# Performance work log

Measured on AMD Instinct MI355X. Metric: run time of the kernel, lower is better.

Reference implementation:

```python
import jax, jax.numpy as jnp
import numpy as np

D = 1024

def setup_inputs() -> dict:
    key = jax.random.key(0)
    ks = jax.random.split(key, 12)
    B, N, d = 4, 4096, D
    init_std = 0.02 / np.sqrt(d)  # matches _init_weights for value_proj / o_proj
    inp = {
        "h": jax.random.normal(ks[0], (B, N, d), dtype=jnp.float32),
        # relation_encoder: Linear(d, d//2) -> GELU -> Linear(d//2, 1)  (weights stored [in, out])
        "W_re1": jax.random.normal(ks[1], (d, d // 2), dtype=jnp.float32) * 0.02,
        "b_re1": jnp.zeros((d // 2,), dtype=jnp.float32),
        "W_re2": jax.random.normal(ks[2], (d // 2, 1), dtype=jnp.float32) * 0.02,
        "b_re2": jnp.zeros((1,), dtype=jnp.float32),
        # value_proj: Linear(d, d, bias=False), init std = 0.02/sqrt(d)
        "W_v": jax.random.normal(ks[3], (d, d), dtype=jnp.float32) * init_std,
        # relation_transform: Linear(2d, d) -> GELU -> Linear(d, d)
        "W_rt1": jax.random.normal(ks[4], (2 * d, d), dtype=jnp.float32) * 0.02,
        "b_rt1": jnp.zeros((d,), dtype=jnp.float32),
        "W_rt2": jax.random.normal(ks[5], (d, d), dtype=jnp.float32) * 0.02,
        "b_rt2": jnp.zeros((d,), dtype=jnp.float32),
        # o_proj: Linear(d, d, bias=False), init std = 0.02/sqrt(d)
        "W_o": jax.random.normal(ks[6], (d, d), dtype=jnp.float32) * init_std,
    }
    return inp


def reference(h, W_re1, b_re1, W_re2, b_re2, W_v, W_rt1, b_rt1, W_rt2, b_rt2, W_o):
    B, N, d = h.shape
    # relation_encoder MLP -> scalar logit per token (torch GELU is exact erf form)
    hidden = jax.nn.gelu(jnp.einsum('bnd,dk->bnk', h, W_re1) + b_re1, approximate=False)
    relation_logits = (jnp.einsum('bnk,ko->bno', hidden, W_re2) + b_re2)[..., 0]  # [B, N]
    relation_strength = jax.nn.sigmoid(relation_logits)  # [B, N]
    # pointer targets: round(sigmoid * (N-1)) clamped (jnp.round == torch.round, half-to-even)
    relation_targets = jnp.clip(
        jnp.round(relation_strength * (N - 1)).astype(jnp.int32), 0, N - 1
    )  # [B, N]
    # per-token gather of target hidden state within each batch row
    target_features = jnp.take_along_axis(h, relation_targets[..., None], axis=1)  # [B, N, d]
    source_values = jnp.einsum('bnd,de->bne', h, W_v)
    target_values = jnp.einsum('bnd,de->bne', target_features, W_v)
    relation_input = jnp.concatenate([source_values, target_values], axis=-1)  # [B, N, 2d]
    relation_output = jax.nn.gelu(
        jnp.einsum('bnf,fe->bne', relation_input, W_rt1) + b_rt1, approximate=False
    )
    relation_output = jnp.einsum('bne,ef->bnf', relation_output, W_rt2) + b_rt2
    z = jnp.einsum('bnd,de->bne', relation_output, W_o)  # [B, N, d]
    return (z, relation_targets, relation_strength)
```

## Files before the change

kernel.cpp:

```cpp
#include <hip/hip_runtime.h>
#include <math.h>
#include <type_traits>

#define DMODEL 1024
#define NSEQ   4096
#define MTOT   16384

typedef unsigned short ushortT;
typedef __attribute__((ext_vector_type(8))) short short8;
typedef __attribute__((ext_vector_type(4))) float f32x4;

__device__ __forceinline__ float gelu_f(float x) {
    return 0.5f * x * (1.0f + erff(x * 0.70710678118654752440f));
}
__device__ __forceinline__ double gelu_d(double x) {
    return 0.5 * x * (1.0 + erf(x * 0.70710678118654752440));
}
__device__ __forceinline__ ushortT f2bf(float f) {
    unsigned u = __float_as_uint(f);
    u += 0x7FFFu + ((u >> 16) & 1u);
    return (ushortT)(u >> 16);
}
__device__ __forceinline__ float bf2f(ushortT b) {
    return __uint_as_float(((unsigned)b) << 16);
}
__device__ __forceinline__ void gload16(const void* g, void* l) {
    __builtin_amdgcn_global_load_lds(
        (const __attribute__((address_space(1))) unsigned*)g,
        (__attribute__((address_space(3))) unsigned*)l, 16, 0, 0);
}

enum { EPI_BIAS_F32 = 2, EPI_TRANS_BF16 = 3, EPI_PQ = 5 };

__device__ __forceinline__ int swz_off(int row, int slot) {
    return row * 64 + (((slot ^ (row & 7)) & 7) << 3);
}

template<int EPI, int NXT>
__global__ __launch_bounds__(512, 2)
void pipe_gemm(const ushortT* __restrict__ A, const ushortT* __restrict__ Bt,
               const float* __restrict__ bias, void* __restrict__ Cv,
               void* __restrict__ Cv2, int K, int lda, int ldb, int ldc, int cpx)
{
    __shared__ ushortT smem[4 * 16384];
    const int tid  = threadIdx.x;
    const int lane = tid & 63;
    const int w    = tid >> 6;
    const int wr   = w >> 2;
    const int wc   = w & 3;
    const int flat = blockIdx.x + blockIdx.y * NXT;
    const int swz  = (flat & 7) * cpx + (flat >> 3);
    const int n0   = (swz & (NXT - 1)) * 256;
    const int m0   = (swz / NXT) * 256;

    const int srow  = tid >> 3;
    const int sscol = (((tid & 7) ^ (srow & 7)) & 7) << 3;

#define STG_A(buf, q, k0) gload16(A  + (size_t)(m0 + (q)*64 + srow) * lda + (k0) + sscol, \
                                  (char*)smem + (buf)*32768 + (q)*8192 + w*1024)
#define STG_B(buf, q, k0) gload16(Bt + (size_t)(n0 + (q)*64 + srow) * ldb + (k0) + sscol, \
                                  (char*)smem + 65536 + (buf)*32768 + (q)*8192 + w*1024)
#define BAR() asm volatile("s_barrier" ::: "memory")

    f32x4 acc[8][4];
    #pragma unroll
    for (int i = 0; i < 8; i++)
        #pragma unroll
        for (int j = 0; j < 4; j++) acc[i][j] = (f32x4){0.f, 0.f, 0.f, 0.f};

    const int NT = K >> 6;

    #pragma unroll
    for (int q = 0; q < 4; q++) { STG_A(0, q, 0); STG_B(0, q, 0); }

    const int mi = lane & 15;
    const int g4 = lane >> 4;

    for (int t = 0; t < NT; ++t) {
        const int c  = t & 1;
        const int nb = c ^ 1;
        const int kn = (t + 1) << 6;
        const bool hn = (t + 1 < NT);

        if (hn) {
            STG_A(nb, 0, kn); STG_A(nb, 1, kn);
            asm volatile("s_waitcnt vmcnt(2)" ::: "memory");
        } else {
            asm volatile("s_waitcnt vmcnt(0)" ::: "memory");
        }
        BAR();

        short8 bf[4][2];
        #pragma unroll
        for (int nf = 0; nf < 4; nf++)
            #pragma unroll
            for (int ks = 0; ks < 2; ks++)
                bf[nf][ks] = *(const short8*)&smem[32768 + c * 16384 +
                                swz_off(wc * 64 + nf * 16 + mi, ks * 4 + g4)];

        #pragma unroll
        for (int p = 0; p < 4; p++) {
            if (p > 0) {
                if (hn) {
                    if (p == 1) { STG_A(nb, 2, kn); STG_A(nb, 3, kn); }
                    if (p == 2) { STG_B(nb, 0, kn); STG_B(nb, 1, kn); }
                    if (p == 3) { STG_B(nb, 2, kn); STG_B(nb, 3, kn); }
                }
                BAR();
            }
            short8 af[2][2];
            #pragma unroll
            for (int ii = 0; ii < 2; ii++)
                #pragma unroll
                for (int ks = 0; ks < 2; ks++)
                    af[ii][ks] = *(const short8*)&smem[c * 16384 +
                                    swz_off(wr * 128 + (p * 2 + ii) * 16 + mi, ks * 4 + g4)];
            __builtin_amdgcn_s_setprio(1);
            #pragma unroll
            for (int ks = 0; ks < 2; ks++)
                #pragma unroll
                for (int ii = 0; ii < 2; ii++)
                    #pragma unroll
                    for (int nf = 0; nf < 4; nf++)
                        acc[p * 2 + ii][nf] = __builtin_amdgcn_mfma_f32_16x16x32_bf16(
                            af[ii][ks], bf[nf][ks], acc[p * 2 + ii][nf], 0, 0, 0);
            __builtin_amdgcn_s_setprio(0);
        }
        BAR();
    }

    const int cr = (lane >> 4) * 4;
    #pragma unroll
    for (int i = 0; i < 8; i++) {
        #pragma unroll
        for (int j = 0; j < 4; j++) {
            const int gr = m0 + wr * 128 + i * 16 + cr;
            const int gc = n0 + wc * 64 + j * 16 + mi;
            #pragma unroll
            for (int r = 0; r < 4; r++) {
                float v = acc[i][j][r];
                if constexpr (EPI == EPI_BIAS_F32) {
                    ((float*)Cv)[(size_t)(gr + r) * ldc + gc] = v + bias[gc];
                } else {
                    if (gc < 1024)
                        ((float*)Cv)[(size_t)(gr + r) * ldc + gc] = v + bias[gc];
                    else
                        ((ushortT*)Cv2)[(size_t)(gr + r) * ldc + (gc - 1024)] = f2bf(v);
                }
            }
        }
    }
#undef STG_A
#undef STG_B
#undef BAR
}

template<int EPI, int NXT>
__global__ __launch_bounds__(256)
void mfma_gemm(const ushortT* __restrict__ A, const ushortT* __restrict__ Bt,
               const float* __restrict__ bias, void* __restrict__ Cv,
               void* __restrict__ Cv2, int K, int lda, int ldb, int ldc, int cpx)
{
    __shared__ ushortT As[128 * 32];
    __shared__ ushortT Bs[128 * 32];
    const int tid  = threadIdx.x;
    const int lane = tid & 63;
    const int w    = tid >> 6;
    const int wr   = (w >> 1) * 64;
    const int wc   = (w & 1) * 64;
    const int flat = blockIdx.x + blockIdx.y * NXT;
    const int swz  = (flat & 7) * cpx + (flat >> 3);
    const int n0   = (swz & (NXT - 1)) * 128;
    const int m0   = (swz / NXT) * 128;

    const int lrow = lane >> 2;
    const int lk   = (lane & 3) * 8;

    f32x4 acc[4][4];
    #pragma unroll
    for (int i = 0; i < 4; i++)
        #pragma unroll
        for (int j = 0; j < 4; j++) acc[i][j] = (f32x4){0.f, 0.f, 0.f, 0.f};

    for (int kk = 0; kk < K; kk += 32) {
        #pragma unroll
        for (int i = 0; i < 2; i++) {
            const ushortT* ga = A + (size_t)(m0 + w * 32 + i * 16 + lrow) * lda + kk + lk;
            gload16(ga, &As[(w * 32 + i * 16) * 32]);
            const ushortT* gb = Bt + (size_t)(n0 + w * 32 + i * 16 + lrow) * ldb + kk + lk;
            gload16(gb, &Bs[(w * 32 + i * 16) * 32]);
        }
        __syncthreads();

        const int mi = lane & 15;
        const int ko = (lane >> 4) * 8;
        short8 a[4], b[4];
        #pragma unroll
        for (int i = 0; i < 4; i++)
            a[i] = *(const short8*)&As[(wr + i * 16 + mi) * 32 + ko];
        #pragma unroll
        for (int j = 0; j < 4; j++)
            b[j] = *(const short8*)&Bs[(wc + j * 16 + mi) * 32 + ko];
        #pragma unroll
        for (int i = 0; i < 4; i++)
            #pragma unroll
            for (int j = 0; j < 4; j++)
                acc[i][j] = __builtin_amdgcn_mfma_f32_16x16x32_bf16(a[i], b[j], acc[i][j], 0, 0, 0);
        __syncthreads();
    }

    const int cr = (lane >> 4) * 4;
    const int cc = lane & 15;
    #pragma unroll
    for (int i = 0; i < 4; i++) {
        #pragma unroll
        for (int j = 0; j < 4; j++) {
            const int gr = m0 + wr + i * 16 + cr;
            const int gc = n0 + wc + j * 16 + cc;
            #pragma unroll
            for (int r = 0; r < 4; r++) {
                float v = acc[i][j][r];
                if constexpr (EPI == EPI_BIAS_F32)
                    ((float*)Cv)[(size_t)(gr + r) * ldc + gc] = v + bias[gc];
                else
                    ((ushortT*)Cv)[(size_t)gc * ldc + (gr + r)] = f2bf(v);
            }
        }
    }
}

__global__ __launch_bounds__(256)
void gelu_gather_k(const float* __restrict__ P, const ushortT* __restrict__ Q,
                   const int* __restrict__ gidx, ushortT* __restrict__ G)
{
    const int m = blockIdx.x;
    int t = gidx[m];
    t = max(0, min(t, MTOT - 1));
    const int c = threadIdx.x * 4;
    float4 p = *(const float4*)(P + (size_t)m * DMODEL + c);
    ushort4 q = *(const ushort4*)(Q + (size_t)t * DMODEL + c);
    ushortT o[4];
    o[0] = f2bf(gelu_f(p.x + bf2f(q.x)));
    o[1] = f2bf(gelu_f(p.y + bf2f(q.y)));
    o[2] = f2bf(gelu_f(p.z + bf2f(q.z)));
    o[3] = f2bf(gelu_f(p.w + bf2f(q.w)));
    *(ulong1*)(G + (size_t)m * DMODEL + c) = *(ulong1*)o;
}

__global__ __launch_bounds__(256)
void wsplit_gemm(const ushortT* __restrict__ Ah, const ushortT* __restrict__ Al,
                 const ushortT* __restrict__ Bh0, const ushortT* __restrict__ Bl0,
                 ushortT* __restrict__ Ct0, int K, int lda, int ldb, int ldc)
{
    __shared__ ushortT Ash[128 * 32], Asl[128 * 32];
    __shared__ ushortT Bsh[128 * 32], Bsl[128 * 32];
    const int tid  = threadIdx.x;
    const int lane = tid & 63;
    const int w    = tid >> 6;
    const int wr   = (w >> 1) * 64;
    const int wc   = (w & 1) * 64;
    const int sel  = blockIdx.y >> 3;
    const int m0   = (blockIdx.y & 7) * 128;
    const int n0   = blockIdx.x * 128;
    const ushortT* Bh = Bh0 + sel * 1024;
    const ushortT* Bl = Bl0 + sel * 1024;
    ushortT* Ct = Ct0 + (size_t)sel * 1024 * 1024;
    const int lrow = lane >> 2;
    const int lk   = (lane & 3) * 8;

    f32x4 acc[4][4];
    #pragma unroll
    for (int i = 0; i < 4; i++)
        #pragma unroll
        for (int j = 0; j < 4; j++) acc[i][j] = (f32x4){0.f, 0.f, 0.f, 0.f};

    for (int kk = 0; kk < K; kk += 32) {
        #pragma unroll
        for (int i = 0; i < 2; i++) {
            const size_t aoff = (size_t)(m0 + w * 32 + i * 16 + lrow) * lda + kk + lk;
            const size_t boff = (size_t)(n0 + w * 32 + i * 16 + lrow) * ldb + kk + lk;
            const int ldst = (w * 32 + i * 16) * 32;
            gload16(Ah + aoff, &Ash[ldst]);
            gload16(Al + aoff, &Asl[ldst]);
            gload16(Bh + boff, &Bsh[ldst]);
            gload16(Bl + boff, &Bsl[ldst]);
        }
        __syncthreads();

        const int mi = lane & 15;
        const int ko = (lane >> 4) * 8;
        short8 ah[4], al[4], bh[4], bl[4];
        #pragma unroll
        for (int i = 0; i < 4; i++) {
            ah[i] = *(const short8*)&Ash[(wr + i * 16 + mi) * 32 + ko];
            al[i] = *(const short8*)&Asl[(wr + i * 16 + mi) * 32 + ko];
        }
        #pragma unroll
        for (int j = 0; j < 4; j++) {
            bh[j] = *(const short8*)&Bsh[(wc + j * 16 + mi) * 32 + ko];
            bl[j] = *(const short8*)&Bsl[(wc + j * 16 + mi) * 32 + ko];
        }
        #pragma unroll
        for (int i = 0; i < 4; i++)
            #pragma unroll
            for (int j = 0; j < 4; j++) {
                acc[i][j] = __builtin_amdgcn_mfma_f32_16x16x32_bf16(ah[i], bh[j], acc[i][j], 0, 0, 0);
                acc[i][j] = __builtin_amdgcn_mfma_f32_16x16x32_bf16(ah[i], bl[j], acc[i][j], 0, 0, 0);
                acc[i][j] = __builtin_amdgcn_mfma_f32_16x16x32_bf16(al[i], bh[j], acc[i][j], 0, 0, 0);
            }
        __syncthreads();
    }

    const int cr = (lane >> 4) * 4;
    const int cc = lane & 15;
    #pragma unroll
    for (int i = 0; i < 4; i++)
        #pragma unroll
        for (int j = 0; j < 4; j++) {
            const int gr = m0 + wr + i * 16 + cr;
            const int gc = n0 + wc + j * 16 + cc;
            #pragma unroll
            for (int r = 0; r < 4; r++)
                Ct[(size_t)gc * ldc + (gr + r)] = f2bf(acc[i][j][r]);
        }
}

__global__ __launch_bounds__(256)
void enc_gemm(const ushortT* __restrict__ Ah, const ushortT* __restrict__ Al,
              const ushortT* __restrict__ Bh, const ushortT* __restrict__ Bl,
              const float* __restrict__ bias, float* __restrict__ C)
{
    __shared__ ushortT Ash[128 * 32], Asl[128 * 32];
    __shared__ ushortT Bsh[128 * 32], Bsl[128 * 32];
    const int tid  = threadIdx.x;
    const int lane = tid & 63;
    const int w    = tid >> 6;
    const int wr   = (w >> 1) * 64;
    const int wc   = (w & 1) * 64;
    const int flat = blockIdx.x + (blockIdx.y << 2);
    const int swz  = (flat & 7) * 64 + (flat >> 3);
    const int n0   = (swz & 3) * 128;
    const int m0   = (swz >> 2) * 128;
    const int lrow = lane >> 2;
    const int lk   = (lane & 3) * 8;

    f32x4 acc[4][4];
    #pragma unroll
    for (int i = 0; i < 4; i++)
        #pragma unroll
        for (int j = 0; j < 4; j++) acc[i][j] = (f32x4){0.f, 0.f, 0.f, 0.f};

    for (int kk = 0; kk < DMODEL; kk += 32) {
        #pragma unroll
        for (int i = 0; i < 2; i++) {
            const size_t aoff = (size_t)(m0 + w * 32 + i * 16 + lrow) * DMODEL + kk + lk;
            const size_t boff = (size_t)(n0 + w * 32 + i * 16 + lrow) * DMODEL + kk + lk;
            const int ldst = (w * 32 + i * 16) * 32;
            gload16(Ah + aoff, &Ash[ldst]);
            gload16(Al + aoff, &Asl[ldst]);
            gload16(Bh + boff, &Bsh[ldst]);
            gload16(Bl + boff, &Bsl[ldst]);
        }
        __syncthreads();

        const int mi = lane & 15;
        const int ko = (lane >> 4) * 8;
        short8 ah[4], al[4], bh[4], bl[4];
        #pragma unroll
        for (int i = 0; i < 4; i++) {
            ah[i] = *(const short8*)&Ash[(wr + i * 16 + mi) * 32 + ko];
            al[i] = *(const short8*)&Asl[(wr + i * 16 + mi) * 32 + ko];
        }
        #pragma unroll
        for (int j = 0; j < 4; j++) {
            bh[j] = *(const short8*)&Bsh[(wc + j * 16 + mi) * 32 + ko];
            bl[j] = *(const short8*)&Bsl[(wc + j * 16 + mi) * 32 + ko];
        }
        #pragma unroll
        for (int i = 0; i < 4; i++)
            #pragma unroll
            for (int j = 0; j < 4; j++) {
                acc[i][j] = __builtin_amdgcn_mfma_f32_16x16x32_bf16(ah[i], bh[j], acc[i][j], 0, 0, 0);
                acc[i][j] = __builtin_amdgcn_mfma_f32_16x16x32_bf16(ah[i], bl[j], acc[i][j], 0, 0, 0);
                acc[i][j] = __builtin_amdgcn_mfma_f32_16x16x32_bf16(al[i], bh[j], acc[i][j], 0, 0, 0);
            }
        __syncthreads();
    }

    const int cr = (lane >> 4) * 4;
    const int cc = lane & 15;
    #pragma unroll
    for (int i = 0; i < 4; i++)
        #pragma unroll
        for (int j = 0; j < 4; j++) {
            const int gr = m0 + wr + i * 16 + cr;
            const int gc = n0 + wc + j * 16 + cc;
            #pragma unroll
            for (int r = 0; r < 4; r++)
                C[(size_t)(gr + r) * 512 + gc] = gelu_f(acc[i][j][r] + bias[gc]);
        }
}

__global__ __launch_bounds__(256)
void target2_k(const float* __restrict__ Genc, const float* __restrict__ W2,
               const float* __restrict__ b2, float* __restrict__ outT,
               float* __restrict__ outS, int* __restrict__ gidx,
               int* __restrict__ cnt, int* __restrict__ list)
{
    const int m = blockIdx.x * 4 + (threadIdx.x >> 6);
    const int lane = threadIdx.x & 63;
    const float* gr = Genc + (size_t)m * 512;
    double s = 0.0;
    #pragma unroll 4
    for (int j = lane; j < 512; j += 64) s = fma((double)gr[j], (double)W2[j], s);
    #pragma unroll
    for (int off = 32; off; off >>= 1) s += __shfl_down(s, off);
    if (lane == 0) {
        double logit = s + (double)b2[0];
        double str = 1.0 / (1.0 + exp(-logit));
        double r = str * (double)(NSEQ - 1);
        double n = rint(r);
        double dist = fabs(r - n);
        n = fmin(fmax(n, 0.0), (double)(NSEQ - 1));
        int t = (int)n;
        outT[m] = (float)t;
        outS[m] = (float)str;
        gidx[m] = ((m >> 12) << 12) + t;
        if (dist > 0.46) {
            int ix = atomicAdd(cnt, 1) & (MTOT - 1);
            list[ix] = m;
        }
    }
}

#define FIX_T 4
__global__ __launch_bounds__(256)
void fixup_k(const float* __restrict__ h, const float* __restrict__ W1,
             const float* __restrict__ b1, const float* __restrict__ W2,
             const float* __restrict__ b2, const int* __restrict__ cnt_p,
             const int* __restrict__ list, float* __restrict__ outT,
             float* __restrict__ outS, int* __restrict__ gidx)
{
    __shared__ float hrow[FIX_T][1024];
    __shared__ double red[4][FIX_T];
    const int tid = threadIdx.x;
    const int cnt = min(*cnt_p, MTOT);
    for (int base = (int)blockIdx.x * FIX_T; base < cnt;
         base += (int)gridDim.x * FIX_T) {
        const int nt = min(FIX_T, cnt - base);
        for (int t = 0; t < nt; t++) {
            const int m = list[base + t];
            const float4* src = (const float4*)(h + (size_t)m * 1024);
            ((float4*)hrow[t])[tid] = src[tid];
        }
        __syncthreads();

        double a[FIX_T][2];
        #pragma unroll
        for (int t = 0; t < FIX_T; t++) { a[t][0] = 0.0; a[t][1] = 0.0; }

        #pragma unroll 4
        for (int k = 0; k < 1024; k++) {
            const double wa = (double)W1[(size_t)k * 512 + tid];
            const double wb = (double)W1[(size_t)k * 512 + tid + 256];
            #pragma unroll
            for (int t = 0; t < FIX_T; t++) {
                const double hv = (double)hrow[t][k];
                a[t][0] = fma(hv, wa, a[t][0]);
                a[t][1] = fma(hv, wb, a[t][1]);
            }
        }

        const double w2a = (double)W2[tid], w2b = (double)W2[tid + 256];
        const double b1a = (double)b1[tid], b1b = (double)b1[tid + 256];
        const int lane = tid & 63, w = tid >> 6;
        #pragma unroll
        for (int t = 0; t < FIX_T; t++) {
            double v = w2a * gelu_d(a[t][0] + b1a) + w2b * gelu_d(a[t][1] + b1b);
            #pragma unroll
            for (int off = 32; off; off >>= 1) v += __shfl_down(v, off);
            if (lane == 0) red[w][t] = v;
        }
        __syncthreads();
        if (tid < nt) {
            const int t = tid;
            double logit = red[0][t] + red[1][t] + red[2][t] + red[3][t] + (double)b2[0];
            double str = 1.0 / (1.0 + exp(-logit));
            double r = str * (double)(NSEQ - 1);
            double n = rint(r);
            n = fmin(fmax(n, 0.0), (double)(NSEQ - 1));
            const int m = list[base + t];
            const int ti = (int)n;
            outT[m] = (float)ti;
            outS[m] = (float)str;
            gidx[m] = ((m >> 12) << 12) + ti;
        }
        __syncthreads();
    }
}

__global__ __launch_bounds__(256)
void biascomb_k(const float* __restrict__ brt2, const float* __restrict__ Wo,
                float* __restrict__ bc)
{
    int j = blockIdx.x * 256 + threadIdx.x;
    float s = 0.f;
    for (int e = 0; e < DMODEL; e++) s = fmaf(brt2[e], Wo[e * DMODEL + j], s);
    bc[j] = s;
}

__global__ __launch_bounds__(256)
void cast_k(const float* __restrict__ x, ushortT* __restrict__ y, int n)
{
    int i = (blockIdx.x * 256 + threadIdx.x) * 4;
    if (i < n) {
        float4 v = *(const float4*)(x + i);
        ushortT o[4] = { f2bf(v.x), f2bf(v.y), f2bf(v.z), f2bf(v.w) };
        *(ulong1*)&y[i] = *(ulong1*)o;
    }
}

__global__ __launch_bounds__(256)
void split_cast_k(const float* __restrict__ x, ushortT* __restrict__ yh,
                  ushortT* __restrict__ yl, int n)
{
    int i = (blockIdx.x * 256 + threadIdx.x) * 4;
    if (i < n) {
        float4 v = *(const float4*)(x + i);
        float vv[4] = { v.x, v.y, v.z, v.w };
        ushortT oh[4], ol[4];
        #pragma unroll
        for (int q = 0; q < 4; q++) {
            oh[q] = f2bf(vv[q]);
            ol[q] = f2bf(vv[q] - bf2f(oh[q]));
        }
        *(ulong1*)&yh[i] = *(ulong1*)oh;
        *(ulong1*)&yl[i] = *(ulong1*)ol;
    }
}

__global__ __launch_bounds__(256)
void transcast_k(const float* __restrict__ W, ushortT* __restrict__ Wt, int K, int N)
{
    __shared__ float t[32][33];
    const int tx = threadIdx.x & 31, ty = threadIdx.x >> 5;
    const int n0 = blockIdx.x * 32, k0 = blockIdx.y * 32;
    #pragma unroll
    for (int r = 0; r < 32; r += 8)
        t[ty + r][tx] = W[(size_t)(k0 + ty + r) * N + n0 + tx];
    __syncthreads();
    #pragma unroll
    for (int r = 0; r < 32; r += 8)
        Wt[(size_t)(n0 + ty + r) * K + k0 + tx] = f2bf(t[tx][ty + r]);
}

__global__ __launch_bounds__(256)
void split_transcast_k(const float* __restrict__ W, ushortT* __restrict__ Wth,
                       ushortT* __restrict__ Wtl, int K, int N)
{
    __shared__ float t[32][33];
    const int tx = threadIdx.x & 31, ty = threadIdx.x >> 5;
    const int n0 = blockIdx.x * 32, k0 = blockIdx.y * 32;
    #pragma unroll
    for (int r = 0; r < 32; r += 8)
        t[ty + r][tx] = W[(size_t)(k0 + ty + r) * N + n0 + tx];
    __syncthreads();
    #pragma unroll
    for (int r = 0; r < 32; r += 8) {
        float x = t[tx][ty + r];
        ushortT hi = f2bf(x);
        Wth[(size_t)(n0 + ty + r) * K + k0 + tx] = hi;
        Wtl[(size_t)(n0 + ty + r) * K + k0 + tx] = f2bf(x - bf2f(hi));
    }
}

extern "C" void kernel_launch(void* const* d_in, const int* in_sizes, int n_in,
                              void* d_out, int out_size, void* d_ws, size_t ws_size,
                              hipStream_t stream)
{
    const float* h     = (const float*)d_in[0];
    const float* W_re1 = (const float*)d_in[1];
    const float* b_re1 = (const float*)d_in[2];
    const float* W_re2 = (const float*)d_in[3];
    const float* b_re2 = (const float*)d_in[4];
    const float* W_v   = (const float*)d_in[5];
    const float* W_rt1 = (const float*)d_in[6];
    const float* b_rt1 = (const float*)d_in[7];
    const float* W_rt2 = (const float*)d_in[8];
    const float* b_rt2 = (const float*)d_in[9];
    const float* W_o   = (const float*)d_in[10];

    float* z    = (float*)d_out;
    float* outT = z + (size_t)MTOT * DMODEL;
    float* outS = outT + MTOT;
    ushortT* Q    = (ushortT*)z;
    ushortT* h_hi = (ushortT*)z + (size_t)MTOT * DMODEL;

    char* ws = (char*)d_ws;
    ushortT* G       = (ushortT*)ws;
    float*   Genc    = (float*)(ws + (32ull  << 20));
    ushortT* h_lo    = (ushortT*)(ws + (64ull  << 20));
    float*   P       = (float*)(ws + (32ull  << 20));
    ushortT* Wrt1t_h = (ushortT*)(ws + (96ull  << 20));
    ushortT* Wrt1t_l = (ushortT*)(ws + (100ull << 20));
    ushortT* Wv_h    = (ushortT*)(ws + (104ull << 20));
    ushortT* Wv_l    = (ushortT*)(ws + (106ull << 20));
    ushortT* Wa_t    = (ushortT*)(ws + (108ull << 20));
    ushortT* Wo_t    = (ushortT*)(ws + (112ull << 20));
    ushortT* Wrt2_b  = (ushortT*)(ws + (114ull << 20));
    ushortT* Wc_t    = (ushortT*)(ws + (116ull << 20));
    ushortT* Wre1t_h = (ushortT*)(ws + (118ull << 20));
    ushortT* Wre1t_l = (ushortT*)(ws + (119ull << 20));
    float*   b_c     = (float*)(ws + (120ull << 20));
    int*     cnt     = (int*)  (ws + (120ull << 20) + 4096);
    int*     gidx    = (int*)  (ws + (120ull << 20) + 8192);
    int*     list    = (int*)  (ws + (120ull << 20) + 8192 + 65536);

    split_cast_k<<<dim3(MTOT * DMODEL / 1024), 256, 0, stream>>>(h, h_hi, h_lo, MTOT * DMODEL);
    split_cast_k<<<dim3(DMODEL * DMODEL / 1024), 256, 0, stream>>>(W_v, Wv_h, Wv_l, DMODEL * DMODEL);
    split_transcast_k<<<dim3(16, 32), 256, 0, stream>>>(W_re1, Wre1t_h, Wre1t_l, DMODEL, 512);
    split_transcast_k<<<dim3(32, 64), 256, 0, stream>>>(W_rt1, Wrt1t_h, Wrt1t_l, 2 * DMODEL, DMODEL);
    cast_k<<<dim3(DMODEL * DMODEL / 1024), 256, 0, stream>>>(W_rt2, Wrt2_b, DMODEL * DMODEL);
    transcast_k<<<dim3(32, 32), 256, 0, stream>>>(W_o, Wo_t, DMODEL, DMODEL);
    biascomb_k<<<dim3(4), 256, 0, stream>>>(b_rt2, W_o, b_c);

    wsplit_gemm<<<dim3(8, 16), 256, 0, stream>>>(Wv_h, Wv_l, Wrt1t_h, Wrt1t_l,
                                                 Wa_t, DMODEL, DMODEL, 2 * DMODEL, DMODEL);

    enc_gemm<<<dim3(4, 128), 256, 0, stream>>>(h_hi, h_lo, Wre1t_h, Wre1t_l, b_re1, Genc);

    hipMemsetAsync(cnt, 0, 4, stream);
    target2_k<<<dim3(MTOT / 4), 256, 0, stream>>>(Genc, W_re2, b_re2, outT, outS, gidx, cnt, list);
    fixup_k<<<dim3(4096), 256, 0, stream>>>(h, W_re1, b_re1, W_re2, b_re2, cnt, list,
                                            outT, outS, gidx);

    mfma_gemm<EPI_TRANS_BF16, 8><<<dim3(8, 8), 256, 0, stream>>>(
        Wrt2_b, Wo_t, nullptr, (void*)Wc_t, nullptr, DMODEL, DMODEL, DMODEL, DMODEL, 8);

    pipe_gemm<EPI_PQ, 8><<<dim3(8, 64), 512, 0, stream>>>(
        h_hi, Wa_t, b_rt1, (void*)P, (void*)Q, DMODEL, DMODEL, DMODEL, DMODEL, 64);

    gelu_gather_k<<<dim3(MTOT), 256, 0, stream>>>(P, Q, gidx, G);

    pipe_gemm<EPI_BIAS_F32, 4><<<dim3(4, 64), 512, 0, stream>>>(
        G, Wc_t, b_c, (void*)z, nullptr, DMODEL, DMODEL, DMODEL, DMODEL, 32);
}
```

Before: 589.6 us.

## Split fixup K-reduction across four thread groups in 1024-thread blocks

The fp64 fixup kernel that recomputes borderline relation targets now uses 1024-thread blocks. Four groups each handle a quarter of the K dimension, and their partial sums are combined through shared memory before the GELU and the dot product with W2. This shortens the serial 1024-long fp64 FMA chain per thread so each flagged token finishes with lower latency. The cost is a larger shared-memory footprint (about 64KB of partial sums), an extra barrier, and fewer blocks in the grid.

```diff
diff --git a/kernel.cpp b/kernel.cpp
--- a/kernel.cpp
+++ b/kernel.cpp
@@ -434,57 +434,74 @@
 }
 
 #define FIX_T 4
-__global__ __launch_bounds__(256)
+__global__ __launch_bounds__(1024)
 void fixup_k(const float* __restrict__ h, const float* __restrict__ W1,
              const float* __restrict__ b1, const float* __restrict__ W2,
              const float* __restrict__ b2, const int* __restrict__ cnt_p,
              const int* __restrict__ list, float* __restrict__ outT,
              float* __restrict__ outS, int* __restrict__ gidx)
 {
-    __shared__ float hrow[FIX_T][1024];
-    __shared__ double red[4][FIX_T];
+    __shared__ float  hrow[FIX_T][1024];
+    __shared__ double part[FIX_T][4][512];
+    __shared__ double red[FIX_T][8];
     const int tid = threadIdx.x;
+    const int kg  = tid >> 8;
+    const int jj  = tid & 255;
     const int cnt = min(*cnt_p, MTOT);
     for (int base = (int)blockIdx.x * FIX_T; base < cnt;
          base += (int)gridDim.x * FIX_T) {
         const int nt = min(FIX_T, cnt - base);
         for (int t = 0; t < nt; t++) {
             const int m = list[base + t];
-            const float4* src = (const float4*)(h + (size_t)m * 1024);
-            ((float4*)hrow[t])[tid] = src[tid];
-        }
-        __syncthreads();
-
-        double a[FIX_T][2];
-        #pragma unroll
-        for (int t = 0; t < FIX_T; t++) { a[t][0] = 0.0; a[t][1] = 0.0; }
-
+            hrow[t][tid] = h[(size_t)m * 1024 + tid];
+        }
+        __syncthreads();
+
+        double a0[FIX_T], a1[FIX_T];
+        #pragma unroll
+        for (int t = 0; t < FIX_T; t++) { a0[t] = 0.0; a1[t] = 0.0; }
+        const int kbase = kg * 256;
         #pragma unroll 4
-        for (int k = 0; k < 1024; k++) {
-            const double wa = (double)W1[(size_t)k * 512 + tid];
-            const double wb = (double)W1[(size_t)k * 512 + tid + 256];
+        for (int kk = 0; kk < 256; kk++) {
+            const int k = kbase + kk;
+            const double wa = (double)W1[(size_t)k * 512 + jj];
+            const double wb = (double)W1[(size_t)k * 512 + jj + 256];
             #pragma unroll
             for (int t = 0; t < FIX_T; t++) {
                 const double hv = (double)hrow[t][k];
-                a[t][0] = fma(hv, wa, a[t][0]);
-                a[t][1] = fma(hv, wb, a[t][1]);
+                a0[t] = fma(hv, wa, a0[t]);
+                a1[t] = fma(hv, wb, a1[t]);
             }
         }
-
-        const double w2a = (double)W2[tid], w2b = (double)W2[tid + 256];
-        const double b1a = (double)b1[tid], b1b = (double)b1[tid + 256];
-        const int lane = tid & 63, w = tid >> 6;
         #pragma unroll
         for (int t = 0; t < FIX_T; t++) {
-            double v = w2a * gelu_d(a[t][0] + b1a) + w2b * gelu_d(a[t][1] + b1b);
-            #pragma unroll
-            for (int off = 32; off; off >>= 1) v += __shfl_down(v, off);
-            if (lane == 0) red[w][t] = v;
+            part[t][kg][jj]       = a0[t];
+            part[t][kg][jj + 256] = a1[t];
+        }
+        __syncthreads();
+
+        if (tid < 512) {
+            const int col  = tid;
+            const int lane = tid & 63;
+            const int wv   = tid >> 6;
+            const double b1c = (double)b1[col];
+            const double w2c = (double)W2[col];
+            #pragma unroll
+            for (int t = 0; t < FIX_T; t++) {
+                double hid = part[t][0][col] + part[t][1][col]
+                           + part[t][2][col] + part[t][3][col] + b1c;
+                double v = gelu_d(hid) * w2c;
+                #pragma unroll
+                for (int off = 32; off; off >>= 1) v += __shfl_down(v, off);
+                if (lane == 0) red[t][wv] = v;
+            }
         }
         __syncthreads();
         if (tid < nt) {
             const int t = tid;
-            double logit = red[0][t] + red[1][t] + red[2][t] + red[3][t] + (double)b2[0];
+            double logit = (double)b2[0];
+            #pragma unroll
+            for (int q = 0; q < 8; q++) logit += red[t][q];
             double str = 1.0 / (1.0 + exp(-logit));
             double r = str * (double)(NSEQ - 1);
             double n = rint(r);
@@ -631,8 +648,8 @@
 
     hipMemsetAsync(cnt, 0, 4, stream);
     target2_k<<<dim3(MTOT / 4), 256, 0, stream>>>(Genc, W_re2, b_re2, outT, outS, gidx, cnt, list);
-    fixup_k<<<dim3(4096), 256, 0, stream>>>(h, W_re1, b_re1, W_re2, b_re2, cnt, list,
-                                            outT, outS, gidx);
+    fixup_k<<<dim3(1024), 1024, 0, stream>>>(h, W_re1, b_re1, W_re2, b_re2, cnt, list,
+                                             outT, outS, gidx);
 
     mfma_gemm<EPI_TRANS_BF16, 8><<<dim3(8, 8), 256, 0, stream>>>(
         Wrt2_b, Wo_t, nullptr, (void*)Wc_t, nullptr, DMODEL, DMODEL, DMODEL, DMODEL, 8);
```

Result: no change. 584.0 us (-1.0%).
